# Optimization experiments

Measured on AMD Instinct MI355X. Metric: run time of the kernel, lower is better.

Reference implementation:

```python
import jax, jax.numpy as jnp
import numpy as np

TAU = 0.01
RHO = 1.99
SIGMA = 1.0 / TAU / 72.0  # 1/tau/72 as in __init__
N_IT = 10  # n_it_max


def nabla2(x):
    # forward finite differences: channel 0 along W (last axis), channel 1 along H
    u = jnp.zeros(x.shape + (2,), x.dtype)
    u = u.at[..., :, :-1, 0].add(x[..., :, 1:] - x[..., :, :-1])
    u = u.at[..., :-1, :, 1].add(x[..., 1:, :] - x[..., :-1, :])
    return u


def nabla2_adjoint(u):
    x = jnp.zeros(u.shape[:-1], u.dtype)
    x = x.at[..., :, :-1].add(-u[..., :, :-1, 0])
    x = x.at[..., :, 1:].add(u[..., :, :-1, 0])
    x = x.at[..., :-1, :].add(-u[..., :-1, :, 1])
    x = x.at[..., 1:, :].add(u[..., :-1, :, 1])
    return x


def epsilon2(I):
    # Jacobian of the vector field I [..., H, W, 2] -> G [..., H, W, 4]
    I0, I1 = I[..., 0], I[..., 1]
    G = jnp.zeros(I0.shape + (4,), I.dtype)
    G = G.at[..., 0].add(I0)                                  # G0 = I0 - shift_H(I0)
    G = G.at[..., 1:, :, 0].add(-I0[..., :-1, :])
    G = G.at[..., :, 1:, 1].add(I0[..., :, 1:] - I0[..., :, :-1])  # G1: W-diff of I0
    G = G.at[..., 2].add(I1)                                  # G2 = I1 - shift_W(I1)
    G = G.at[..., :, 1:, 2].add(-I1[..., :, :-1])
    G = G.at[..., :-1, :, 3].add(I1[..., 1:, :] - I1[..., :-1, :])  # G3: H-diff of I1
    return G


def epsilon2_adjoint(G):
    I = jnp.zeros(G.shape[:-1] + (2,), G.dtype)
    I = I.at[..., 0].add(G[..., 0])
    I = I.at[..., :-1, :, 0].add(-G[..., 1:, :, 0])
    I = I.at[..., :, :-1, 0].add(-G[..., :, 1:, 1])
    I = I.at[..., :, 1:, 0].add(G[..., :, 1:, 1])
    I = I.at[..., 1].add(G[..., 2])
    I = I.at[..., :, :-1, 1].add(-G[..., :, 1:, 2])
    I = I.at[..., :-1, :, 1].add(-G[..., :-1, :, 3])
    I = I.at[..., 1:, :, 1].add(G[..., :-1, :, 3])
    return I


def setup_inputs() -> dict:
    key = jax.random.key(0)
    y = jax.random.normal(key, (4, 512, 512), dtype=jnp.float32)
    return {"y": y, "ths": 1}


def reference(y, ths):
    lam1 = ths * 0.1
    lam2 = ths * 0.15

    def prox_tau_fr(r):
        left = jnp.sqrt(jnp.sum(r * r, axis=-1)) / (TAU * lam1)
        return r - r / jnp.maximum(left, 1.0)[..., None]

    def prox_sigma_g_conj(u):
        return u / jnp.maximum(jnp.sqrt(jnp.sum(u * u, axis=-1)) / lam2, 1.0)[..., None]

    x2 = y
    r2 = jnp.zeros(y.shape + (2,), y.dtype)
    u2 = jnp.zeros(y.shape + (4,), y.dtype)

    def step(carry, _):
        x2, r2, u2 = carry
        tmp = TAU * epsilon2_adjoint(u2)
        x = (x2 - nabla2_adjoint(tmp) + TAU * y) / (1.0 + TAU)  # prox_tau_fx
        r = prox_tau_fr(r2 + tmp)
        u = prox_sigma_g_conj(
            u2 + SIGMA * epsilon2(nabla2(2.0 * x - x2) - (2.0 * r - r2))
        )
        x2 = x2 + RHO * (x - x2)
        r2 = r2 + RHO * (r - r2)
        u2 = u2 + RHO * (u - u2)
        return (x2, r2, u2), None

    (x2, r2, u2), _ = jax.lax.scan(step, (x2, r2, u2), None, length=N_IT)
    return x2
```

## Files before the change

### kernel.cpp

```cpp
#include <hip/hip_runtime.h>
#include <hip/hip_fp16.h>
#include <math.h>

#define HH 512
#define WW 512
#define BB 4
#define NPIX (BB * HH * WW)

#define HS 4
#define NSX 9
#define NBAND (HH / HS)
#define NWAVES (NSX * NBAND * BB)
#define NBLK (NWAVES / 4)

constexpr float TAUf   = 0.01f;
constexpr float RHOf   = 1.99f;
constexpr float SIGMAf = (float)(1.0 / 0.01 / 72.0);
constexpr float INV1PT = (float)(1.0 / 1.01);

__device__ __forceinline__ float SD(float v) { return __shfl_down(v, 1, 64); }
__device__ __forceinline__ unsigned SDu(unsigned v) { return __shfl_down(v, 1, 64); }
__device__ __forceinline__ float SUp(float v) { return __shfl_up(v, 1, 64); }


template <int MODE>
__global__ __launch_bounds__(256) void sweep(
    const float* __restrict__ y, const int* __restrict__ ths_p,
    const uint2* __restrict__ f_in, const uint2* __restrict__ u_in,
    uint2* __restrict__ f_out, uint2* __restrict__ u_out,
    float* __restrict__ xout)
{
    const int tid  = threadIdx.x;
    const int lane = tid & 63;
    const int wid  = blockIdx.x * 4 + (tid >> 6);
    const int sx   = wid % NSX;
    const int t2   = wid / NSX;
    const int band = t2 & (NBAND - 1);
    const int b    = t2 / NBAND;
    const int R0   = band * HS;
    const int w    = sx * 60 - 2 + lane;
    const int boff = b * (HH * WW);
    const bool wok = ((unsigned)w) < (unsigned)WW;
    const float mA = (w >= 1 && w < WW) ? 1.f : 0.f;
    const float mB = (w >= 0 && w < WW - 1) ? 1.f : 0.f;
    const bool cok = (lane >= 2) && (lane < 62) && (w < WW);

    const float ths  = (float)ths_p[0];
    const float tl1_ = TAUf * (ths * 0.1f);
    const float l2_  = ths * 0.15f;

    float uf0[4], uf1[4], uf2[4], uf3[4];
    unsigned u12r[4];
    float i0r[2], i1r[2];
    float sr[2], t1r[2];
    float v0r[4], v1r[2];
    #pragma unroll
    for (int q = 0; q < 4; ++q) { uf0[q]=uf1[q]=uf2[q]=uf3[q]=0.f; v0r[q]=0.f; u12r[q]=0u; }
    i0r[0]=i0r[1]=i1r[0]=i1r[1]=0.f;
    sr[0]=sr[1]=0.f; t1r[0]=t1r[1]=0.f; v1r[0]=v1r[1]=0.f;

    auto uload = [&](int row) -> uint2 {
        uint2 z; z.x = 0u; z.y = 0u;
        if (((unsigned)row) < (unsigned)HH && wok)
            z = u_in[(size_t)(boff + row * WW + w)];
        return z;
    };
    auto fload = [&](int row) -> uint2 {
        uint2 z; z.x = 0u; z.y = 0u;
        if (((unsigned)row) < (unsigned)HH && wok)
            z = f_in[(size_t)(boff + row * WW + w)];
        return z;
    };
    auto unpk = [&](int slot, uint2 raw) {
        __half2 lo = *(reinterpret_cast<__half2*>(&raw.x));
        __half2 hi = *(reinterpret_cast<__half2*>(&raw.y));
        uf0[slot] = __low2float(lo); uf1[slot] = __high2float(lo);
        uf2[slot] = __low2float(hi); uf3[slot] = __high2float(hi);
        u12r[slot] = (raw.x >> 16) | (raw.y << 16);
    };
    auto compI = [&](int rr, int islot, int c, int d, int uu_) {
        if (((unsigned)rr) < (unsigned)HH) {
            float hD  = (rr < HH - 1) ? 1.f : 0.f;
            unsigned pp = SDu(u12r[c]);
            __half2 ph = *(reinterpret_cast<__half2*>(&pp));
            float u1n = __low2float(ph);
            float u2n = __high2float(ph);
            i0r[islot] = uf0[c] - uf0[d] - u1n + mA * uf1[c];
            i1r[islot] = uf2[c] - u2n - hD * uf3[c] + uf3[uu_];
        } else { i0r[islot] = 0.f; i1r[islot] = 0.f; }
    };

    if (MODE == 2) {
        unpk(2, uload(R0 - 2));
        unpk(3, uload(R0 - 1));
        unpk(0, uload(R0));
        compI(R0 - 1, 1, 3, 0, 2);
        uint2 puA = uload(R0 + 1);
        uint2 puB = uload(R0 + 2);
        uint2 pfA = fload(R0);
        uint2 pfB = fload(R0 + 1);
        #pragma unroll
        for (int k = 0; k < HS; ++k) {
            const int rr = R0 + k;
            unpk((k + 1) & 3, puA);
            puA = puB;
            if (k < HS - 2) puB = uload(R0 + k + 3);
            __half2 lo = *(reinterpret_cast<__half2*>(&pfA.x));
            __half2 hi = *(reinterpret_cast<__half2*>(&pfA.y));
            float x2v = __low2float(lo);
            float yv  = __high2float(hi);
            pfA = pfB;
            if (k < HS - 2) pfB = fload(R0 + k + 2);
            compI(rr, k & 1, k & 3, (k + 1) & 3, (k + 3) & 3);
            float hD = (rr < HH - 1) ? 1.f : 0.f;
            float i0c = i0r[k & 1], i1c = i1r[k & 1], i1u = i1r[(k + 1) & 1];
            float i0l = SUp(i0c);
            float na = TAUf * (mA * i0l - mB * i0c + i1u - hD * i1c);
            float x = (x2v - na + TAUf * yv) * INV1PT;
            if (cok) xout[boff + rr * WW + w] = x2v + RHOf * (x - x2v);
        }
        return;
    }

    auto compS = [&](int rr, int isc, int isp,
                     float yv, float x2v, float r20v, float r21v, unsigned yraw,
                     bool coreRow, float &sOut, float &t0Out, float &t1Out) {
        if (((unsigned)rr) < (unsigned)HH) {
            float hD = (rr < HH - 1) ? 1.f : 0.f;
            float i0c = i0r[isc], i1c = i1r[isc], i1u = i1r[isp];
            float i0l = SUp(i0c);
            float na = TAUf * (mA * i0l - mB * i0c + i1u - hD * i1c);
            float x = (x2v - na + TAUf * yv) * INV1PT;
            float rr0 = r20v + TAUf * i0c;
            float rr1 = r21v + TAUf * i1c;
            float d = rr0 * rr0 + rr1 * rr1;
            float rinv = fminf(tl1_ * __builtin_amdgcn_rsqf(d), 1.0f);
            float r0 = rr0 - rr0 * rinv;
            float r1 = rr1 - rr1 * rinv;
            sOut  = 2.f * x  - x2v;
            t0Out = 2.f * r0 - r20v;
            t1Out = 2.f * r1 - r21v;
            if (coreRow && cok) {
                int idx = boff + rr * WW + w;
                __half2 lo2 = __floats2half2_rn(x2v + RHOf * (x - x2v),
                                                r20v + RHOf * (r0 - r20v));
                unsigned r1b = (unsigned)__half_as_ushort(
                    __float2half(r21v + RHOf * (r1 - r21v)));
                uint2 st; st.x = *(unsigned*)&lo2; st.y = r1b | (yraw << 16);
                f_out[(size_t)idx] = st;
            }
        } else { sOut = 0.f; t0Out = 0.f; t1Out = 0.f; }
    };

    auto compU = [&](int ro, int v0c_s, int v0u_s, int v1c_s, int v1d_s, int uslot) {
        float hD  = (ro < HH - 1) ? 1.f : 0.f;
        float v0c = v0r[v0c_s], v0u = v0r[v0u_s];
        float v1c = v1r[v1c_s], v1d = v1r[v1d_s];
        float v0l = SUp(v0c);
        float v1l = SUp(v1c);
        float G0 = v0c - v0u;
        float G1 = mA * (v0c - v0l);
        float G2 = v1c - mA * v1l;
        float G3 = hD * (v1d - v1c);
        float u0v = uf0[uslot], u1v = uf1[uslot], u2v = uf2[uslot], u3v = uf3[uslot];
        float uu0 = u0v + SIGMAf * G0;
        float uu1 = u1v + SIGMAf * G1;
        float uu2 = u2v + SIGMAf * G2;
        float uu3 = u3v + SIGMAf * G3;
        float d = uu0 * uu0 + uu1 * uu1 + uu2 * uu2 + uu3 * uu3;
        float ui = fminf(l2_ * __builtin_amdgcn_rsqf(d), 1.0f);
        if (cok) {
            int idx = boff + ro * WW + w;
            __half2 lo = __floats2half2_rn(u0v + RHOf * (uu0 * ui - u0v),
                                           u1v + RHOf * (uu1 * ui - u1v));
            __half2 hi = __floats2half2_rn(u2v + RHOf * (uu2 * ui - u2v),
                                           u3v + RHOf * (uu3 * ui - u3v));
            uint2 st; st.x = *(unsigned*)&lo; st.y = *(unsigned*)&hi;
            u_out[(size_t)idx] = st;
        }
    };

    uint2 puA, puB, pfA, pfB;
    puA.x = puA.y = puB.x = puB.y = 0u;
    pfA.x = pfA.y = pfB.x = pfB.y = 0u;
    unpk(1, uload(R0 - 3));
    unpk(2, uload(R0 - 2));
    unpk(3, uload(R0 - 1));
    compI(R0 - 2, 0, 2, 3, 1);
    puA = uload(R0);
    puB = uload(R0 + 1);
    pfA = fload(R0 - 1);
    pfB = fload(R0);

    #pragma unroll
    for (int k = 0; k < HS + 3; ++k) {
        const int rr = R0 - 1 + k;
        unpk(k & 3, puA);
        puA = puB;
        if (k <= HS) puB = uload(R0 + k + 2);
        __half2 lo = *(reinterpret_cast<__half2*>(&pfA.x));
        __half2 hi = *(reinterpret_cast<__half2*>(&pfA.y));
        float x2v  = __low2float(lo);
        float r20v = __high2float(lo);
        float r21v = __low2float(hi);
        float yv   = __high2float(hi);
        unsigned yraw = pfA.y >> 16;
        pfA = pfB;
        if (k <= HS) pfB = fload(R0 + k + 1);

        compI(rr, (k + 1) & 1, (k + 3) & 3, k & 3, (k + 2) & 3);

        float sN, t0N, t1N;
        compS(rr, (k + 1) & 1, k & 1, yv, x2v, r20v, r21v, yraw,
              (k >= 1 && k <= HS), sN, t0N, t1N);

        {
            float sPrev  = sr[k & 1];
            float t1Prev = t1r[k & 1];
            float hDm1   = (rr < HH) ? 1.f : 0.f;
            v0r[(k + 3) & 3] = mB * (SD(sN) - sN) - t0N;
            v1r[k & 1]       = hDm1 * (sN - sPrev) - t1Prev;
            sr[(k + 1) & 1]  = sN;
            t1r[(k + 1) & 1] = t1N;
        }

        if (k >= 3) compU(R0 - 3 + k, (k + 1) & 3, k & 3, (k + 1) & 1, k & 1,
                          (k + 1) & 3);
    }
}

__global__ __launch_bounds__(256) void fused01(
    const float* __restrict__ y, const int* __restrict__ ths_p,
    uint2* __restrict__ f_out, uint2* __restrict__ u_out)
{
    const int tid  = threadIdx.x;
    const int lane = tid & 63;
    const int wid  = blockIdx.x * 4 + (tid >> 6);
    const int sx   = wid % NSX;
    const int t2   = wid / NSX;
    const int band = t2 & (NBAND - 1);
    const int b    = t2 / NBAND;
    const int R0   = band * HS;
    const int w    = sx * 58 - 3 + lane;
    const int boff = b * (HH * WW);
    const bool wok = ((unsigned)w) < (unsigned)WW;
    const float mA = (w >= 1 && w < WW) ? 1.f : 0.f;
    const float mB = (w >= 0 && w < WW - 1) ? 1.f : 0.f;
    const bool cok = (lane >= 3) && (lane <= 60) && (w < WW);

    const float ths  = (float)ths_p[0];
    const float tl1_ = TAUf * (ths * 0.1f);
    const float l2_  = ths * 0.15f;

    float p0r[4];
    float p1r[2];
    float yD1 = 0.f, yD2 = 0.f, yD3 = 0.f;

    float uf0[4], uf1[4], uf2[4], uf3[4];
    unsigned u12r[4];
    float i0r[2], i1r[2];
    float sr[2], t1r[2];
    float v0r[4], v1r[2];
    #pragma unroll
    for (int q = 0; q < 4; ++q) {
        uf0[q]=uf1[q]=uf2[q]=uf3[q]=0.f; v0r[q]=0.f; u12r[q]=0u; p0r[q]=0.f;
    }
    i0r[0]=i0r[1]=i1r[0]=i1r[1]=0.f;
    sr[0]=sr[1]=0.f; t1r[0]=t1r[1]=0.f; v1r[0]=v1r[1]=0.f; p1r[0]=p1r[1]=0.f;

    auto yload = [&](int row) -> float {
        return (((unsigned)row) < (unsigned)HH && wok)
                   ? y[boff + row * WW + w] : 0.f;
    };
    auto unpk = [&](int slot, uint2 raw) {
        __half2 lo = *(reinterpret_cast<__half2*>(&raw.x));
        __half2 hi = *(reinterpret_cast<__half2*>(&raw.y));
        uf0[slot] = __low2float(lo); uf1[slot] = __high2float(lo);
        uf2[slot] = __low2float(hi); uf3[slot] = __high2float(hi);
        u12r[slot] = (raw.x >> 16) | (raw.y << 16);
    };
    auto compI = [&](int rr, int islot, int c, int d, int uu_) {
        if (((unsigned)rr) < (unsigned)HH) {
            float hD  = (rr < HH - 1) ? 1.f : 0.f;
            unsigned pp = SDu(u12r[c]);
            __half2 ph = *(reinterpret_cast<__half2*>(&pp));
            float u1n = __low2float(ph);
            float u2n = __high2float(ph);
            i0r[islot] = uf0[c] - uf0[d] - u1n + mA * uf1[c];
            i1r[islot] = uf2[c] - u2n - hD * uf3[c] + uf3[uu_];
        } else { i0r[islot] = 0.f; i1r[islot] = 0.f; }
    };

    float pyA = yload(R0 - 4);
    float pyB = yload(R0 - 3);

    #pragma unroll
    for (int j = 0; j < HS + 9; ++j) {
        const int p = R0 - 4 + j;
        float yp = pyA; pyA = pyB;
        if (j <= HS + 6) pyB = yload(R0 - 2 + j);

        p0r[j & 3]       = mB * (SD(yp) - yp);
        p1r[(j + 1) & 1] = ((p < HH) ? 1.f : 0.f) * (yp - yD1);

        if (j >= 3) {
            const int ro = R0 - 6 + j;
            float hD  = (ro < HH - 1) ? 1.f : 0.f;
            float v0c = p0r[(j + 2) & 3], v0u = p0r[(j + 1) & 3];
            float v1c = p1r[j & 1],       v1d = p1r[(j + 1) & 1];
            float G0 = v0c - v0u;
            float G1 = mA * (v0c - SUp(v0c));
            float G2 = v1c - mA * SUp(v1c);
            float G3 = hD * (v1d - v1c);
            float uu0 = SIGMAf * G0, uu1 = SIGMAf * G1;
            float uu2 = SIGMAf * G2, uu3 = SIGMAf * G3;
            float d = uu0*uu0 + uu1*uu1 + uu2*uu2 + uu3*uu3;
            float ui = fminf(l2_ * __builtin_amdgcn_rsqf(d), 1.0f);
            __half2 lo = __floats2half2_rn(RHOf * (uu0 * ui), RHOf * (uu1 * ui));
            __half2 hi = __floats2half2_rn(RHOf * (uu2 * ui), RHOf * (uu3 * ui));
            uint2 st; st.x = *(unsigned*)&lo; st.y = *(unsigned*)&hi;
            unpk((j + 2) & 3, st);
        }

        if (j == 5) compI(R0 - 2, 0, 2, 3, 1);

        if (j >= 6) {
            const int k  = j - 6;
            const int rr = R0 - 1 + k;
            __half yh = __float2half(yD3);
            float yv  = __half2float(yh);
            unsigned yraw = (unsigned)__half_as_ushort(yh);

            compI(rr, (k + 1) & 1, (k + 3) & 3, k & 3, (k + 2) & 3);

            float sN, t0N, t1N;
            {
                const bool coreRow = (k >= 1 && k <= HS);
                if (((unsigned)rr) < (unsigned)HH) {
                    float hD = (rr < HH - 1) ? 1.f : 0.f;
                    float i0c = i0r[(k + 1) & 1], i1c = i1r[(k + 1) & 1];
                    float i1u = i1r[k & 1];
                    float i0l = SUp(i0c);
                    float na = TAUf * (mA * i0l - mB * i0c + i1u - hD * i1c);
                    float x = (yv - na + TAUf * yv) * INV1PT;
                    float rr0 = TAUf * i0c;
                    float rr1 = TAUf * i1c;
                    float d2 = rr0*rr0 + rr1*rr1;
                    float rinv = fminf(tl1_ * __builtin_amdgcn_rsqf(d2), 1.0f);
                    float r0 = rr0 - rr0 * rinv;
                    float r1 = rr1 - rr1 * rinv;
                    sN  = 2.f * x - yv;
                    t0N = 2.f * r0;
                    t1N = 2.f * r1;
                    if (coreRow && cok) {
                        int idx = boff + rr * WW + w;
                        __half2 lo2 = __floats2half2_rn(yv + RHOf * (x - yv),
                                                        RHOf * r0);
                        unsigned r1b = (unsigned)__half_as_ushort(
                            __float2half(RHOf * r1));
                        uint2 st2; st2.x = *(unsigned*)&lo2;
                        st2.y = r1b | (yraw << 16);
                        f_out[(size_t)idx] = st2;
                    }
                } else { sN = 0.f; t0N = 0.f; t1N = 0.f; }
            }

            {
                float sPrev  = sr[k & 1];
                float t1Prev = t1r[k & 1];
                float hDm1   = (rr < HH) ? 1.f : 0.f;
                v0r[(k + 3) & 3] = mB * (SD(sN) - sN) - t0N;
                v1r[k & 1]       = hDm1 * (sN - sPrev) - t1Prev;
                sr[(k + 1) & 1]  = sN;
                t1r[(k + 1) & 1] = t1N;
            }

            if (k >= 3) {
                const int ro = R0 - 3 + k;
                float hD  = (ro < HH - 1) ? 1.f : 0.f;
                float v0c = v0r[(k + 1) & 3], v0u = v0r[k & 3];
                float v1c = v1r[(k + 1) & 1], v1d = v1r[k & 1];
                float v0l = SUp(v0c);
                float v1l = SUp(v1c);
                float G0 = v0c - v0u;
                float G1 = mA * (v0c - v0l);
                float G2 = v1c - mA * v1l;
                float G3 = hD * (v1d - v1c);
                const int us = (k + 1) & 3;
                float u0v = uf0[us], u1v = uf1[us], u2v = uf2[us], u3v = uf3[us];
                float uu0 = u0v + SIGMAf * G0;
                float uu1 = u1v + SIGMAf * G1;
                float uu2 = u2v + SIGMAf * G2;
                float uu3 = u3v + SIGMAf * G3;
                float d = uu0*uu0 + uu1*uu1 + uu2*uu2 + uu3*uu3;
                float ui = fminf(l2_ * __builtin_amdgcn_rsqf(d), 1.0f);
                if (cok) {
                    int idx = boff + ro * WW + w;
                    __half2 lo = __floats2half2_rn(u0v + RHOf * (uu0 * ui - u0v),
                                                   u1v + RHOf * (uu1 * ui - u1v));
                    __half2 hi = __floats2half2_rn(u2v + RHOf * (uu2 * ui - u2v),
                                                   u3v + RHOf * (uu3 * ui - u3v));
                    uint2 st; st.x = *(unsigned*)&lo; st.y = *(unsigned*)&hi;
                    u_out[(size_t)idx] = st;
                }
            }
        }

        yD3 = yD2; yD2 = yD1; yD1 = yp;
    }
}

extern "C" void kernel_launch(void* const* d_in, const int* in_sizes, int n_in,
                              void* d_out, int out_size, void* d_ws, size_t ws_size,
                              hipStream_t stream)
{
    const float* y   = (const float*)d_in[0];
    const int*   ths = (const int*)d_in[1];
    uint2* ws2 = (uint2*)d_ws;

    uint2* FA = ws2;
    uint2* UA = ws2 + (size_t)NPIX;
    uint2* FB = ws2 + 2 * (size_t)NPIX;
    uint2* UB = ws2 + 3 * (size_t)NPIX;
    float* xout = (float*)d_out;

    dim3 block(256);
    dim3 grid(NBLK);

    fused01<<<grid, block, 0, stream>>>(y, ths, FA, UA);
    uint2 *fi = FA, *ui = UA, *fo = FB, *uo = UB;
    for (int it = 2; it <= 8; ++it) {
        sweep<1><<<grid, block, 0, stream>>>(y, ths, fi, ui, fo, uo, nullptr);
        uint2* t;
        t = fi; fi = fo; fo = t;
        t = ui; ui = uo; uo = t;
    }
    sweep<2><<<grid, block, 0, stream>>>(y, ths, fi, ui, nullptr, nullptr, xout);
}
```

Measured before the change: 155.8 us.

## Fuse final two iterations into a single temporally-blocked kernel

Replaces the last full sweep plus final output sweep with one kernel that computes iteration 9's full update and then iteration 10's x-output in the same pass, keeping the intermediate state in registers. This removes one kernel launch and one round trip of the f/u state through global memory. In exchange it adds register pressure and extra halo recomputation in the same 58-column strip, with only the central columns written.

```diff
diff --git a/kernel.cpp b/kernel.cpp
--- a/kernel.cpp
+++ b/kernel.cpp
@@ -410,6 +410,216 @@
     }
 }
 
+__global__ __launch_bounds__(256) void fused89(
+    const int* __restrict__ ths_p,
+    const uint2* __restrict__ f_in, const uint2* __restrict__ u_in,
+    float* __restrict__ xout)
+{
+    const int tid  = threadIdx.x;
+    const int lane = tid & 63;
+    const int wid  = blockIdx.x * 4 + (tid >> 6);
+    const int sx   = wid % NSX;
+    const int t2   = wid / NSX;
+    const int band = t2 & (NBAND - 1);
+    const int b    = t2 / NBAND;
+    const int R0   = band * HS;
+    const int R0p  = R0 - 2;
+    const int w    = sx * 58 - 3 + lane;
+    const int boff = b * (HH * WW);
+    const bool wok = ((unsigned)w) < (unsigned)WW;
+    const float mA = (w >= 1 && w < WW) ? 1.f : 0.f;
+    const float mB = (w >= 0 && w < WW - 1) ? 1.f : 0.f;
+    const bool cokC = (lane >= 3) && (lane <= 60) && (w < WW);
+
+    const float ths  = (float)ths_p[0];
+    const float tl1_ = TAUf * (ths * 0.1f);
+    const float l2_  = ths * 0.15f;
+
+    constexpr int HSp = HS + 3;
+
+    float uf0[4], uf1[4], uf2[4], uf3[4];
+    unsigned u12r[4];
+    float i0r[2], i1r[2];
+    float sr[2], t1r[2];
+    float v0r[4], v1r[2];
+    float cf0[4], cf1[4], cf2[4], cf3[4];
+    unsigned c12[4];
+    float ci0[2], ci1[2];
+    uint2 fmid[4];
+    #pragma unroll
+    for (int q = 0; q < 4; ++q) {
+        uf0[q]=uf1[q]=uf2[q]=uf3[q]=0.f; v0r[q]=0.f; u12r[q]=0u;
+        cf0[q]=cf1[q]=cf2[q]=cf3[q]=0.f; c12[q]=0u;
+        fmid[q].x = 0u; fmid[q].y = 0u;
+    }
+    i0r[0]=i0r[1]=i1r[0]=i1r[1]=0.f;
+    ci0[0]=ci0[1]=ci1[0]=ci1[1]=0.f;
+    sr[0]=sr[1]=0.f; t1r[0]=t1r[1]=0.f; v1r[0]=v1r[1]=0.f;
+
+    auto uload = [&](int row) -> uint2 {
+        uint2 z; z.x = 0u; z.y = 0u;
+        if (((unsigned)row) < (unsigned)HH && wok)
+            z = u_in[(size_t)(boff + row * WW + w)];
+        return z;
+    };
+    auto fload = [&](int row) -> uint2 {
+        uint2 z; z.x = 0u; z.y = 0u;
+        if (((unsigned)row) < (unsigned)HH && wok)
+            z = f_in[(size_t)(boff + row * WW + w)];
+        return z;
+    };
+    auto unpk = [&](int slot, uint2 raw) {
+        __half2 lo = *(reinterpret_cast<__half2*>(&raw.x));
+        __half2 hi = *(reinterpret_cast<__half2*>(&raw.y));
+        uf0[slot] = __low2float(lo); uf1[slot] = __high2float(lo);
+        uf2[slot] = __low2float(hi); uf3[slot] = __high2float(hi);
+        u12r[slot] = (raw.x >> 16) | (raw.y << 16);
+    };
+    auto compI = [&](int rr, int islot, int c, int d, int uu_) {
+        if (((unsigned)rr) < (unsigned)HH) {
+            float hD  = (rr < HH - 1) ? 1.f : 0.f;
+            unsigned pp = SDu(u12r[c]);
+            __half2 ph = *(reinterpret_cast<__half2*>(&pp));
+            float u1n = __low2float(ph);
+            float u2n = __high2float(ph);
+            i0r[islot] = uf0[c] - uf0[d] - u1n + mA * uf1[c];
+            i1r[islot] = uf2[c] - u2n - hD * uf3[c] + uf3[uu_];
+        } else { i0r[islot] = 0.f; i1r[islot] = 0.f; }
+    };
+    auto cunpk = [&](int slot, uint2 raw) {
+        __half2 lo = *(reinterpret_cast<__half2*>(&raw.x));
+        __half2 hi = *(reinterpret_cast<__half2*>(&raw.y));
+        cf0[slot] = __low2float(lo); cf1[slot] = __high2float(lo);
+        cf2[slot] = __low2float(hi); cf3[slot] = __high2float(hi);
+        c12[slot] = (raw.x >> 16) | (raw.y << 16);
+    };
+    auto ccompI = [&](int rr, int islot, int c, int d, int uu_) {
+        if (((unsigned)rr) < (unsigned)HH) {
+            float hD  = (rr < HH - 1) ? 1.f : 0.f;
+            unsigned pp = SDu(c12[c]);
+            __half2 ph = *(reinterpret_cast<__half2*>(&pp));
+            float u1n = __low2float(ph);
+            float u2n = __high2float(ph);
+            ci0[islot] = cf0[c] - cf0[d] - u1n + mA * cf1[c];
+            ci1[islot] = cf2[c] - u2n - hD * cf3[c] + cf3[uu_];
+        } else { ci0[islot] = 0.f; ci1[islot] = 0.f; }
+    };
+
+    unpk(1, uload(R0p - 3));
+    unpk(2, uload(R0p - 2));
+    unpk(3, uload(R0p - 1));
+    compI(R0p - 2, 0, 2, 3, 1);
+    uint2 puA = uload(R0p);
+    uint2 puB = uload(R0p + 1);
+    uint2 pfA = fload(R0p - 1);
+    uint2 pfB = fload(R0p);
+
+    #pragma unroll
+    for (int J = 0; J < HSp + 3; ++J) {
+        const int rp = R0p - 1 + J;
+
+        unpk(J & 3, puA);
+        puA = puB;
+        if (J <= HSp) puB = uload(R0p + J + 2);
+        __half2 flo = *(reinterpret_cast<__half2*>(&pfA.x));
+        __half2 fhi = *(reinterpret_cast<__half2*>(&pfA.y));
+        float x2v  = __low2float(flo);
+        float r20v = __high2float(flo);
+        float r21v = __low2float(fhi);
+        float yv   = __high2float(fhi);
+        unsigned yraw = pfA.y >> 16;
+        pfA = pfB;
+        if (J <= HSp) pfB = fload(R0p + J + 1);
+
+        compI(rp, (J + 1) & 1, (J + 3) & 3, J & 3, (J + 2) & 3);
+
+        float sN, t0N, t1N;
+        if (((unsigned)rp) < (unsigned)HH) {
+            float hD = (rp < HH - 1) ? 1.f : 0.f;
+            float i0c = i0r[(J + 1) & 1], i1c = i1r[(J + 1) & 1];
+            float i1u = i1r[J & 1];
+            float i0l = SUp(i0c);
+            float na = TAUf * (mA * i0l - mB * i0c + i1u - hD * i1c);
+            float x = (x2v - na + TAUf * yv) * INV1PT;
+            float rr0 = r20v + TAUf * i0c;
+            float rr1 = r21v + TAUf * i1c;
+            float d = rr0 * rr0 + rr1 * rr1;
+            float rinv = fminf(tl1_ * __builtin_amdgcn_rsqf(d), 1.0f);
+            float r0 = rr0 - rr0 * rinv;
+            float r1 = rr1 - rr1 * rinv;
+            sN  = 2.f * x  - x2v;
+            t0N = 2.f * r0 - r20v;
+            t1N = 2.f * r1 - r21v;
+            if (J >= 3 && J <= HS + 2) {
+                __half2 lo2 = __floats2half2_rn(x2v + RHOf * (x - x2v),
+                                                r20v + RHOf * (r0 - r20v));
+                unsigned r1b = (unsigned)__half_as_ushort(
+                    __float2half(r21v + RHOf * (r1 - r21v)));
+                uint2 st; st.x = *(unsigned*)&lo2; st.y = r1b | (yraw << 16);
+                fmid[(J + 1) & 3] = st;
+            }
+        } else { sN = 0.f; t0N = 0.f; t1N = 0.f; }
+
+        {
+            float sPrev  = sr[J & 1];
+            float t1Prev = t1r[J & 1];
+            float hDm1   = (rp < HH) ? 1.f : 0.f;
+            v0r[(J + 3) & 3] = mB * (SD(sN) - sN) - t0N;
+            v1r[J & 1]       = hDm1 * (sN - sPrev) - t1Prev;
+            sr[(J + 1) & 1]  = sN;
+            t1r[(J + 1) & 1] = t1N;
+        }
+
+        if (J >= 3) {
+            const int ro = R0p - 3 + J;
+            float hD  = (ro < HH - 1) ? 1.f : 0.f;
+            float v0c = v0r[(J + 1) & 3], v0u = v0r[J & 3];
+            float v1c = v1r[(J + 1) & 1], v1d = v1r[J & 1];
+            float v0l = SUp(v0c);
+            float v1l = SUp(v1c);
+            float G0 = v0c - v0u;
+            float G1 = mA * (v0c - v0l);
+            float G2 = v1c - mA * v1l;
+            float G3 = hD * (v1d - v1c);
+            const int us = (J + 1) & 3;
+            float u0v = uf0[us], u1v = uf1[us], u2v = uf2[us], u3v = uf3[us];
+            float uu0 = u0v + SIGMAf * G0;
+            float uu1 = u1v + SIGMAf * G1;
+            float uu2 = u2v + SIGMAf * G2;
+            float uu3 = u3v + SIGMAf * G3;
+            float d = uu0*uu0 + uu1*uu1 + uu2*uu2 + uu3*uu3;
+            float ui = fminf(l2_ * __builtin_amdgcn_rsqf(d), 1.0f);
+            uint2 st; st.x = 0u; st.y = 0u;
+            if (((unsigned)ro) < (unsigned)HH) {
+                __half2 lo = __floats2half2_rn(u0v + RHOf * (uu0 * ui - u0v),
+                                               u1v + RHOf * (uu1 * ui - u1v));
+                __half2 hi = __floats2half2_rn(u2v + RHOf * (uu2 * ui - u2v),
+                                               u3v + RHOf * (uu3 * ui - u3v));
+                st.x = *(unsigned*)&lo; st.y = *(unsigned*)&hi;
+            }
+            cunpk((J + 3) & 3, st);
+        }
+
+        if (J == 5) ccompI(R0 - 1, 1, 3, 0, 2);
+        if (J >= 6) {
+            const int kc = J - 6;
+            const int rc = R0 + kc;
+            ccompI(rc, kc & 1, kc & 3, (kc + 1) & 3, (kc + 3) & 3);
+            uint2 fm = fmid[(J + 2) & 3];
+            __half2 mlo = *(reinterpret_cast<__half2*>(&fm.x));
+            __half2 mhi = *(reinterpret_cast<__half2*>(&fm.y));
+            float cx2 = __low2float(mlo);
+            float cyv = __high2float(mhi);
+            float hD = (rc < HH - 1) ? 1.f : 0.f;
+            float i0c = ci0[kc & 1], i1c = ci1[kc & 1], i1u = ci1[(kc + 1) & 1];
+            float i0l = SUp(i0c);
+            float na = TAUf * (mA * i0l - mB * i0c + i1u - hD * i1c);
+            float x = (cx2 - na + TAUf * cyv) * INV1PT;
+            if (cokC) xout[boff + rc * WW + w] = cx2 + RHOf * (x - cx2);
+        }
+    }
+}
+
 extern "C" void kernel_launch(void* const* d_in, const int* in_sizes, int n_in,
                               void* d_out, int out_size, void* d_ws, size_t ws_size,
                               hipStream_t stream)
@@ -429,11 +639,11 @@
 
     fused01<<<grid, block, 0, stream>>>(y, ths, FA, UA);
     uint2 *fi = FA, *ui = UA, *fo = FB, *uo = UB;
-    for (int it = 2; it <= 8; ++it) {
+    for (int it = 2; it <= 7; ++it) {
         sweep<1><<<grid, block, 0, stream>>>(y, ths, fi, ui, fo, uo, nullptr);
         uint2* t;
         t = fi; fi = fo; fo = t;
         t = ui; ui = uo; uo = t;
     }
-    sweep<2><<<grid, block, 0, stream>>>(y, ths, fi, ui, nullptr, nullptr, xout);
+    fused89<<<grid, block, 0, stream>>>(ths, fi, ui, xout);
 }
```

After: 151.6 us. 1.03x faster.
